# Kernel optimization log

Hardware: AMD Instinct MI355X
Metric: run time of the kernel (lower is better)

The kernel has to match this reference:

```python
import jax, jax.numpy as jnp
import numpy as np

B, CIN, COUT, T, F = 8, 64, 64, 512, 161
KH, KW = 3, 3
PAD_H, PAD_W = 1, 1
STRIDE_H, STRIDE_W = 1, 1
DIL_H, DIL_W = 1, 1


def setup_inputs() -> dict:
    key = jax.random.key(0)
    k1, k2, k3 = jax.random.split(key, 3)
    x = jax.random.normal(k1, (B, CIN, T, F), dtype=jnp.float32)
    # kernel: [out_ch, in_ch, kernels(freq), kH, kW]
    kernel = jax.random.normal(k2, (COUT, CIN, F, KH, KW), dtype=jnp.float32) * 0.05
    bias = jax.random.normal(k3, (1, COUT, 1, F), dtype=jnp.float32) * 0.05
    return {"x": x, "kernel": kernel, "bias": bias}


def reference(x, kernel, bias):
    # Frequency-varying conv: out[b,o,t,f] = sum_{i,m,n} xp[b,i,t*sH+m*dH, f*sW+n*dW] * kernel[o,i,f,m,n] + bias
    xp = jnp.pad(x, ((0, 0), (0, 0), (PAD_H, PAD_H), (PAD_W, PAD_W)))
    Hp, Wp = xp.shape[-2], xp.shape[-1]
    out_t = (Hp - ((KH - 1) * DIL_H + 1)) // STRIDE_H + 1
    out_f = (Wp - ((KW - 1) * DIL_W + 1)) // STRIDE_W + 1  # == F == kernels
    out = jnp.zeros((x.shape[0], kernel.shape[0], out_t, out_f), dtype=x.dtype)
    # Small fixed loop over the 3x3 window; avoids materializing [B,C,T,F,3,3] patches.
    for m in range(KH):
        for n in range(KW):
            xs = xp[:, :,
                    m * DIL_H : m * DIL_H + out_t * STRIDE_H : STRIDE_H,
                    n * DIL_W : n * DIL_W + out_f * STRIDE_W : STRIDE_W]  # [B,Cin,T,F]
            out = out + jnp.einsum('bitf,oif->botf', xs, kernel[:, :, :, m, n])
    out = out + bias
    return out
```

## Files before the change

### kernel.cpp

```cpp
#include <hip/hip_runtime.h>
#include <hip/hip_bf16.h>

#define CIN   64
#define COUT  64
#define TT    512
#define FF    161
#define KTOT  576
#define WST   (COUT*KTOT)
#define TFSTR (TT*FF)
#define FP_   168

#define W2_BYTES  ((size_t)FF*COUT*KTOT*2)
#define X2_BYTES  ((size_t)8*TT*FP_*64*2)
#define TMP_BYTES ((size_t)8*FF*TT*COUT*2)
#define PW_BLOCKS 5796

typedef __bf16 bf16x8 __attribute__((ext_vector_type(8)));
typedef float  f32x4  __attribute__((ext_vector_type(4)));
typedef unsigned short u16x8 __attribute__((ext_vector_type(8)));
typedef unsigned short u16x4 __attribute__((ext_vector_type(4)));
typedef unsigned int   u32x2 __attribute__((ext_vector_type(2)));
typedef float f4u __attribute__((ext_vector_type(4), aligned(4)));

__device__ __forceinline__ unsigned short f2bf(float v) {
    union { float f; unsigned int u; } c; c.f = v;
    unsigned int u = c.u + 0x7FFFu + ((c.u >> 16) & 1u);
    return (unsigned short)(u >> 16);
}
__device__ __forceinline__ float bf2f(unsigned short h) {
    union { unsigned int u; float f; } c; c.u = (unsigned)h << 16;
    return c.f;
}

__global__ __launch_bounds__(256) void prep_fused(
    const float* __restrict__ ksrc, unsigned short* __restrict__ w2,
    const float* __restrict__ x, unsigned short* __restrict__ x2)
{
    __shared__ unsigned short Xs[64][172];
    int bx = blockIdx.x;
    int tid = threadIdx.x;

    if (bx < PW_BLOCKS) {
        int g  = bx*256 + tid;
        int f  = g / 9216;
        int j  = g - f*9216;
        int o  = j / 144;
        int r  = j - o*144;
        int q  = r >> 4;
        int i4 = (r & 15) * 4;
        u16x4 v;
        #pragma unroll
        for (int e = 0; e < 4; ++e)
            v[e] = f2bf(ksrc[((size_t)(o*64 + i4 + e)*FF + f)*9 + q]);
        *(u16x4*)&w2[(size_t)f*36864 + j*4] = v;
        return;
    }

    int bt = bx - PW_BLOCKS;
    int b  = bt >> 9;
    int t  = bt & 511;
    const float* xb = x + (size_t)b*CIN*TFSTR + (size_t)t*FF;
    #pragma unroll
    for (int k = 0; k < 11; ++k) {
        int s = tid + k*256;
        if (s < 2624) {
            int i = s / 41;
            int u = s - i*41;
            const float* p = xb + (size_t)i*TFSTR + 4*u;
            if (u < 40) {
                f4u v = *(const f4u*)p;
                u32x2 pk = { (unsigned)f2bf(v.x) | ((unsigned)f2bf(v.y) << 16),
                             (unsigned)f2bf(v.z) | ((unsigned)f2bf(v.w) << 16) };
                *(u32x2*)&Xs[i][4*u] = pk;
            } else {
                Xs[i][160] = f2bf(*p);
            }
        }
    }
    __syncthreads();
    unsigned short* ob = x2 + (size_t)bt * FP_ * 64;
    #pragma unroll
    for (int k = 0; k < 6; ++k) {
        int s = tid + k*256;
        if (s < 1344) {
            int fp = s >> 3;
            int j  = s & 7;
            u16x8 v = {0,0,0,0,0,0,0,0};
            if (fp >= 1 && fp < 162) {
                int f = fp - 1;
                #pragma unroll
                for (int e = 0; e < 8; ++e) v[e] = Xs[j*8 + e][f];
            }
            *(u16x8*)&ob[fp*64 + j*8] = v;
        }
    }
}

__global__ __launch_bounds__(256, 4) void conv_mfma8(
    const unsigned short* __restrict__ x2, const unsigned short* __restrict__ w2,
    const float* __restrict__ bias, unsigned short* __restrict__ tmp)
{
    int bx   = blockIdx.x;
    int b    = bx & 7;
    int r    = bx >> 3;
    int tq   = r & 7;
    int fblk = r >> 3;
    int t0   = tq * 64;
    int f0   = fblk * 2;

    __shared__ alignas(16) unsigned short As[264*64];

    int tid = threadIdx.x;
    int wq  = tid >> 6;
    int l   = tid & 63;
    int l15 = l & 15;
    int lq  = l >> 4;
    int o   = wq*16 + l15;

    const unsigned short* zrow = x2 + 167*64;

    #pragma unroll
    for (int it = 0; it < 9; ++it) {
        int idx = tid + it*256;
        if (idx < 2112) {
            int row = idx >> 3;
            int j   = idx & 7;
            int fl  = row / 66;
            int tl  = row - fl*66;
            int gt  = t0 - 1 + tl;
            int fp  = f0 + fl;
            bool ok = (gt >= 0) && (gt < TT);
            int key = (tl + fl) & 7;
            const unsigned short* src = ok
                ? x2 + ((((size_t)b*TT + gt)*FP_ + fp)*64 + ((j ^ key) * 8))
                : zrow + j*8;
            __builtin_amdgcn_global_load_lds(
                (const __attribute__((address_space(1))) void*)src,
                (__attribute__((address_space(3))) void*)(As + (size_t)idx*8),
                16, 0, 0);
        }
    }
    __syncthreads();

    f32x4 acc[2][4] = {};
    const unsigned short* wb = w2 + ((size_t)f0*COUT + o)*KTOT;

    bf16x8 bw0[6], bw1[6];
    auto ldw = [&](bf16x8 (&dst)[6], int p) {
        int is = p / 3, dm = p - (p/3)*3;
        int kb = is*32 + lq*8;
        #pragma unroll
        for (int dn = 0; dn < 3; ++dn)
            #pragma unroll
            for (int u = 0; u < 2; ++u)
                dst[dn*2 + u] = *(const bf16x8*)&wb[(size_t)u*WST + (dm*3 + dn)*64 + kb];
    };

    ldw(bw0, 0);
    #pragma unroll
    for (int p = 0; p < 6; ++p) {
        if (p < 5) {
            if (p & 1) ldw(bw0, p + 1); else ldw(bw1, p + 1);
        }
        int is = p / 3, dm = p - (p/3)*3;
        int sbase = is*4 + lq;
        #pragma unroll
        for (int mf = 0; mf < 4; ++mf) {
            int tl = mf*16 + l15 + dm;
            bf16x8 a4[4];
            #pragma unroll
            for (int fl = 0; fl < 4; ++fl) {
                int slot = sbase ^ ((tl + fl) & 7);
                a4[fl] = *(const bf16x8*)&As[(size_t)(fl*66 + tl)*64 + slot*8];
            }
            #pragma unroll
            for (int dn = 0; dn < 3; ++dn)
                #pragma unroll
                for (int u = 0; u < 2; ++u)
                    acc[u][mf] = __builtin_amdgcn_mfma_f32_16x16x32_bf16(
                        a4[u + dn], (p & 1) ? bw1[dn*2 + u] : bw0[dn*2 + u],
                        acc[u][mf], 0, 0, 0);
        }
    }

    #pragma unroll
    for (int u = 0; u < 2; ++u) {
        int fe = f0 + u;
        if (fe < FF) {
            float bv = bias[o*FF + fe];
            size_t tb = ((size_t)b*FF + fe)*TT + t0;
            #pragma unroll
            for (int mf = 0; mf < 4; ++mf)
                #pragma unroll
                for (int rr = 0; rr < 4; ++rr) {
                    int t = mf*16 + lq*4 + rr;
                    tmp[(tb + t)*COUT + o] = f2bf(acc[u][mf][rr] + bv);
                }
        }
    }
}

__global__ __launch_bounds__(256) void finalize2(
    const unsigned short* __restrict__ tmp, float* __restrict__ out)
{
    int bx = blockIdx.x;
    int b  = bx & 7;
    int s  = bx >> 3;
    int tb = s >> 1;
    int oh = s & 1;
    int t0 = tb * 4;
    int o0 = oh * 32;

    __shared__ unsigned short Ld[644*40];

    int tid = threadIdx.x;

    #pragma unroll
    for (int k = 0; k < 11; ++k) {
        int sl = tid + k*256;
        if (sl < 2576) {
            int f = sl >> 4;
            int r = sl & 15;
            int t = r >> 2;
            int j = r & 3;
            const unsigned short* src =
                tmp + (((size_t)b*FF + f)*TT + t0 + t)*COUT + o0 + j*8;
            int row = t*FF + f;
            *(u16x8*)&Ld[row*40 + ((j ^ (f & 3)) << 3)] = *(const u16x8*)src;
        }
    }
    __syncthreads();

    for (int ol = 0; ol < 32; ++ol) {
        int o = o0 + ol;
        float* op = out + (((size_t)b*COUT + o)*TT + t0)*FF;
        int jo = ol >> 3, o7 = ol & 7;
        #pragma unroll
        for (int k = 0; k < 3; ++k) {
            int r = tid + k*256;
            if (r < 4*FF) {
                int f = r % FF;
                op[r] = bf2f(Ld[r*40 + ((jo ^ (f & 3)) << 3) + o7]);
            }
        }
    }
}

__global__ __launch_bounds__(256) void conv_mfma(
    const float* __restrict__ x, const unsigned short* __restrict__ w2,
    const float* __restrict__ bias, float* __restrict__ out)
{
    int bx = blockIdx.x;
    int r  = bx & 7;
    int q  = bx >> 3;
    int fblk = q % 41;
    int g  = (q / 41) * 8 + r;
    int b  = g >> 3;
    int t0 = (g & 7) * 64;
    int f0 = fblk * 4;

    __shared__ unsigned short Bs[6][66][64];
    int tid = threadIdx.x;

    for (int i = 0; i < 64; i += 4) {
        #pragma unroll
        for (int pp = 0; pp < 2; ++pp) {
            int p = tid + pp*256;
            if (p < 396) {
                int tl = p / 6, fl = p % 6;
                int gt = t0 - 1 + tl;
                int gf = f0 - 1 + fl;
                bool ok = (gt >= 0) && (gt < TT) && (gf >= 0) && (gf < FF);
                const float* xp = x + (((size_t)(b*CIN + i)*TT + gt)*FF + gf);
                float v0 = ok ? xp[0]       : 0.f;
                float v1 = ok ? xp[TFSTR]   : 0.f;
                float v2 = ok ? xp[2*TFSTR] : 0.f;
                float v3 = ok ? xp[3*TFSTR] : 0.f;
                int isw = i ^ (((tl + fl) & 7) << 3);
                ushort4 pk;
                pk.x = f2bf(v0); pk.y = f2bf(v1); pk.z = f2bf(v2); pk.w = f2bf(v3);
                *reinterpret_cast<ushort4*>(&Bs[fl][tl][isw]) = pk;
            }
        }
    }
    __syncthreads();

    int wv = tid >> 6;
    int l  = tid & 63;
    int f  = f0 + wv;
    if (f >= FF) return;

    int l15 = l & 15;
    int lq  = l >> 4;
    f32x4 acc[4][4] = {};
    const unsigned short* wb = w2 + (size_t)f * (COUT * KTOT);

    #pragma unroll
    for (int dm = 0; dm < 3; ++dm)
    #pragma unroll
    for (int dn = 0; dn < 3; ++dn) {
        int fl = wv + dn;
        int kq = (dm*3 + dn) * 64;
        #pragma unroll
        for (int is = 0; is < 2; ++is) {
            int i0 = is*32 + lq*8;
            bf16x8 a[4];
            #pragma unroll
            for (int mf = 0; mf < 4; ++mf) {
                int tl  = mf*16 + l15 + dm;
                int isw = i0 ^ (((tl + fl) & 7) << 3);
                a[mf] = *(const bf16x8*)&Bs[fl][tl][isw];
            }
            int kb = kq + i0;
            #pragma unroll
            for (int nf = 0; nf < 4; ++nf) {
                bf16x8 bfr = *(const bf16x8*)&wb[(size_t)(nf*16 + l15) * KTOT + kb];
                #pragma unroll
                for (int mf = 0; mf < 4; ++mf)
                    acc[mf][nf] = __builtin_amdgcn_mfma_f32_16x16x32_bf16(
                        a[mf], bfr, acc[mf][nf], 0, 0, 0);
            }
        }
    }

    #pragma unroll
    for (int nf = 0; nf < 4; ++nf) {
        int o = nf*16 + l15;
        float bv = bias[o*FF + f];
        size_t obase = (((size_t)b*COUT + o)*TT + t0 + lq*4)*FF + f;
        #pragma unroll
        for (int mf = 0; mf < 4; ++mf)
            #pragma unroll
            for (int rr = 0; rr < 4; ++rr)
                out[obase + (size_t)(mf*16 + rr)*FF] = acc[mf][nf][rr] + bv;
    }
}

extern "C" void kernel_launch(void* const* d_in, const int* in_sizes, int n_in,
                              void* d_out, int out_size, void* d_ws, size_t ws_size,
                              hipStream_t stream)
{
    (void)in_sizes; (void)n_in; (void)out_size;
    const float* x    = (const float*)d_in[0];
    const float* k    = (const float*)d_in[1];
    const float* bias = (const float*)d_in[2];
    float* out = (float*)d_out;
    unsigned short* w2  = (unsigned short*)d_ws;
    unsigned short* x2  = (unsigned short*)((char*)d_ws + W2_BYTES);
    unsigned short* tmp = (unsigned short*)((char*)d_ws + W2_BYTES + X2_BYTES);

    bool big2 = (ws_size >= W2_BYTES + X2_BYTES + TMP_BYTES);

    prep_fused<<<big2 ? (PW_BLOCKS + 8*TT) : PW_BLOCKS, 256, 0, stream>>>(k, w2, x, x2);

    if (big2) {
        conv_mfma8<<<5184, 256, 0, stream>>>(x2, w2, bias, tmp);
        finalize2<<<2048, 256, 0, stream>>>(tmp, out);
    } else {
        conv_mfma<<<8*41*8, 256, 0, stream>>>(x, w2, bias, out);
    }
}
```

Baseline: 261.1 us.

## Switch conv to 32x32x16 MFMA tiles and stage weight repack through LDS

The conv kernel now gives each wave one frequency and 32 output channels, and uses 32x32x16 bf16 MFMA over the nine taps, where it used 16x16x32 across two frequencies. This changes the LDS A-fragment reuse and the accumulator layout. The weight-prep blocks now read contiguous rows of the kernel into shared memory and write out the transposed bf16 layout. This replaces scattered strided global reads with far fewer blocks. The larger MFMA shape may shift register pressure and occupancy.

```diff
diff --git a/kernel.cpp b/kernel.cpp
--- a/kernel.cpp
+++ b/kernel.cpp
@@ -13,10 +13,11 @@
 #define W2_BYTES  ((size_t)FF*COUT*KTOT*2)
 #define X2_BYTES  ((size_t)8*TT*FP_*64*2)
 #define TMP_BYTES ((size_t)8*FF*TT*COUT*2)
-#define PW_BLOCKS 5796
+#define PREPW_BLOCKS 512
 
 typedef __bf16 bf16x8 __attribute__((ext_vector_type(8)));
 typedef float  f32x4  __attribute__((ext_vector_type(4)));
+typedef float  f32x16 __attribute__((ext_vector_type(16)));
 typedef unsigned short u16x8 __attribute__((ext_vector_type(8)));
 typedef unsigned short u16x4 __attribute__((ext_vector_type(4)));
 typedef unsigned int   u32x2 __attribute__((ext_vector_type(2)));
@@ -32,31 +33,45 @@
     return c.f;
 }
 
-__global__ __launch_bounds__(256) void prep_fused(
+__global__ __launch_bounds__(256) void prep_fused2(
     const float* __restrict__ ksrc, unsigned short* __restrict__ w2,
     const float* __restrict__ x, unsigned short* __restrict__ x2)
 {
+    __shared__ unsigned short Ls[64*190];
     __shared__ unsigned short Xs[64][172];
     int bx = blockIdx.x;
     int tid = threadIdx.x;
 
-    if (bx < PW_BLOCKS) {
-        int g  = bx*256 + tid;
-        int f  = g / 9216;
-        int j  = g - f*9216;
-        int o  = j / 144;
-        int r  = j - o*144;
-        int q  = r >> 4;
-        int i4 = (r & 15) * 4;
-        u16x4 v;
-        #pragma unroll
-        for (int e = 0; e < 4; ++e)
-            v[e] = f2bf(ksrc[((size_t)(o*64 + i4 + e)*FF + f)*9 + q]);
-        *(u16x4*)&w2[(size_t)f*36864 + j*4] = v;
+    if (bx < PREPW_BLOCKS) {
+        int o  = bx >> 3;
+        int c  = bx & 7;
+        int f0 = c * 21;
+        int nf = (c == 7) ? 14 : 21;
+        int nr = nf * 9;
+        const float* src = ksrc + (size_t)o*64*FF*9 + f0*9;
+        int tot = 64 * nr;
+        for (int e = tid; e < tot; e += 256) {
+            int i  = e / nr;
+            int rr = e - i*nr;
+            Ls[i*190 + rr] = f2bf(src[(size_t)i*FF*9 + rr]);
+        }
+        __syncthreads();
+        unsigned short* dst = w2 + (size_t)f0*WST + o*KTOT;
+        int wt = nf * 144;
+        for (int w = tid; w < wt; w += 256) {
+            int fl = w / 144;
+            int rr = w - fl*144;
+            int q  = rr >> 4;
+            int i0 = (rr & 15) * 4;
+            u16x4 v;
+            #pragma unroll
+            for (int e = 0; e < 4; ++e) v[e] = Ls[(i0 + e)*190 + fl*9 + q];
+            *(u16x4*)&dst[(size_t)fl*WST + q*64 + i0] = v;
+        }
         return;
     }
 
-    int bt = bx - PW_BLOCKS;
+    int bt = bx - PREPW_BLOCKS;
     int b  = bt >> 9;
     int t  = bt & 511;
     const float* xb = x + (size_t)b*CIN*TFSTR + (size_t)t*FF;
@@ -96,7 +111,7 @@
     }
 }
 
-__global__ __launch_bounds__(256, 4) void conv_mfma8(
+__global__ __launch_bounds__(256, 4) void conv_mfma10(
     const unsigned short* __restrict__ x2, const unsigned short* __restrict__ w2,
     const float* __restrict__ bias, unsigned short* __restrict__ tmp)
 {
@@ -113,9 +128,11 @@
     int tid = threadIdx.x;
     int wq  = tid >> 6;
     int l   = tid & 63;
-    int l15 = l & 15;
-    int lq  = l >> 4;
-    int o   = wq*16 + l15;
+    int l31 = l & 31;
+    int lh  = l >> 5;
+    int f   = f0 + (wq >> 1);
+    int o   = (wq & 1)*32 + l31;
+    int flb = wq >> 1;
 
     const unsigned short* zrow = x2 + 167*64;
 
@@ -142,60 +159,45 @@
     }
     __syncthreads();
 
-    f32x4 acc[2][4] = {};
-    const unsigned short* wb = w2 + ((size_t)f0*COUT + o)*KTOT;
-
-    bf16x8 bw0[6], bw1[6];
-    auto ldw = [&](bf16x8 (&dst)[6], int p) {
-        int is = p / 3, dm = p - (p/3)*3;
-        int kb = is*32 + lq*8;
-        #pragma unroll
-        for (int dn = 0; dn < 3; ++dn)
-            #pragma unroll
-            for (int u = 0; u < 2; ++u)
-                dst[dn*2 + u] = *(const bf16x8*)&wb[(size_t)u*WST + (dm*3 + dn)*64 + kb];
+    f32x16 acc0 = {}, acc1 = {};
+    const unsigned short* wb = w2 + ((size_t)f*COUT + o)*KTOT + lh*8;
+
+    bf16x8 bwA[4], bwB[4];
+    auto ldw = [&](bf16x8 (&dst)[4], int t9) {
+        #pragma unroll
+        for (int ks = 0; ks < 4; ++ks)
+            dst[ks] = *(const bf16x8*)&wb[t9*64 + ks*16];
     };
 
-    ldw(bw0, 0);
-    #pragma unroll
-    for (int p = 0; p < 6; ++p) {
-        if (p < 5) {
-            if (p & 1) ldw(bw0, p + 1); else ldw(bw1, p + 1);
-        }
-        int is = p / 3, dm = p - (p/3)*3;
-        int sbase = is*4 + lq;
-        #pragma unroll
-        for (int mf = 0; mf < 4; ++mf) {
-            int tl = mf*16 + l15 + dm;
-            bf16x8 a4[4];
-            #pragma unroll
-            for (int fl = 0; fl < 4; ++fl) {
-                int slot = sbase ^ ((tl + fl) & 7);
-                a4[fl] = *(const bf16x8*)&As[(size_t)(fl*66 + tl)*64 + slot*8];
-            }
-            #pragma unroll
-            for (int dn = 0; dn < 3; ++dn)
-                #pragma unroll
-                for (int u = 0; u < 2; ++u)
-                    acc[u][mf] = __builtin_amdgcn_mfma_f32_16x16x32_bf16(
-                        a4[u + dn], (p & 1) ? bw1[dn*2 + u] : bw0[dn*2 + u],
-                        acc[u][mf], 0, 0, 0);
-        }
-    }
-
-    #pragma unroll
-    for (int u = 0; u < 2; ++u) {
-        int fe = f0 + u;
-        if (fe < FF) {
-            float bv = bias[o*FF + fe];
-            size_t tb = ((size_t)b*FF + fe)*TT + t0;
-            #pragma unroll
-            for (int mf = 0; mf < 4; ++mf)
-                #pragma unroll
-                for (int rr = 0; rr < 4; ++rr) {
-                    int t = mf*16 + lq*4 + rr;
-                    tmp[(tb + t)*COUT + o] = f2bf(acc[u][mf][rr] + bv);
-                }
+    ldw(bwA, 0);
+    #pragma unroll
+    for (int t9 = 0; t9 < 9; ++t9) {
+        if (t9 < 8) { if (t9 & 1) ldw(bwA, t9 + 1); else ldw(bwB, t9 + 1); }
+        int dm = t9 / 3, dn = t9 - dm*3;
+        int fl = flb + dn;
+        #pragma unroll
+        for (int ks = 0; ks < 4; ++ks) {
+            int sb = ks*2 + lh;
+            int tlA = l31 + dm;
+            int slA = sb ^ ((tlA + fl) & 7);
+            bf16x8 a0 = *(const bf16x8*)&As[(size_t)(fl*66 + tlA)*64 + slA*8];
+            int tlB = 32 + l31 + dm;
+            int slB = sb ^ ((tlB + fl) & 7);
+            bf16x8 a1 = *(const bf16x8*)&As[(size_t)(fl*66 + tlB)*64 + slB*8];
+            bf16x8 bw = (t9 & 1) ? bwB[ks] : bwA[ks];
+            acc0 = __builtin_amdgcn_mfma_f32_32x32x16_bf16(a0, bw, acc0, 0, 0, 0);
+            acc1 = __builtin_amdgcn_mfma_f32_32x32x16_bf16(a1, bw, acc1, 0, 0, 0);
+        }
+    }
+
+    if (f < FF) {
+        float bv = bias[o*FF + f];
+        size_t tb = ((size_t)b*FF + f)*TT + t0;
+        #pragma unroll
+        for (int reg = 0; reg < 16; ++reg) {
+            int t = (reg & 3) + 8*(reg >> 2) + 4*lh;
+            tmp[(tb + t)*COUT + o]      = f2bf(acc0[reg] + bv);
+            tmp[(tb + t + 32)*COUT + o] = f2bf(acc1[reg] + bv);
         }
     }
 }
@@ -351,12 +353,12 @@
 
     bool big2 = (ws_size >= W2_BYTES + X2_BYTES + TMP_BYTES);
 
-    prep_fused<<<big2 ? (PW_BLOCKS + 8*TT) : PW_BLOCKS, 256, 0, stream>>>(k, w2, x, x2);
-
     if (big2) {
-        conv_mfma8<<<5184, 256, 0, stream>>>(x2, w2, bias, tmp);
+        prep_fused2<<<PREPW_BLOCKS + 8*TT, 256, 0, stream>>>(k, w2, x, x2);
+        conv_mfma10<<<5184, 256, 0, stream>>>(x2, w2, bias, tmp);
         finalize2<<<2048, 256, 0, stream>>>(tmp, out);
     } else {
+        prep_fused2<<<PREPW_BLOCKS, 256, 0, stream>>>(k, w2, x, x2);
         conv_mfma<<<8*41*8, 256, 0, stream>>>(x, w2, bias, out);
     }
 }
```

Result: slower. 293.4 us (+12.4%).

## Make conv blocks persistent over several frequency pairs with ring-buffered input planes

Applied to the files above, without the earlier changes.

Each conv block now handles 2-3 consecutive frequency pairs instead of one. Input planes sit in a 6-slot LDS ring, so the two planes shared by adjacent pairs are reused and the next pair's planes are prefetched while the current pair computes. This cuts redundant global loads of the overlapping padded-frequency planes and reduces the grid from 5184 to 2048 blocks. In exchange LDS use per block grows, occupancy drops to 3 blocks per CU, and extra barriers are added between iterations.

```diff
diff --git a/kernel.cpp b/kernel.cpp
--- a/kernel.cpp
+++ b/kernel.cpp
@@ -21,6 +21,7 @@
 typedef unsigned short u16x4 __attribute__((ext_vector_type(4)));
 typedef unsigned int   u32x2 __attribute__((ext_vector_type(2)));
 typedef float f4u __attribute__((ext_vector_type(4), aligned(4)));
+typedef float f2u __attribute__((ext_vector_type(2), aligned(4)));
 
 __device__ __forceinline__ unsigned short f2bf(float v) {
     union { float f; unsigned int u; } c; c.f = v;
@@ -96,19 +97,20 @@
     }
 }
 
-__global__ __launch_bounds__(256, 4) void conv_mfma8(
+__global__ __launch_bounds__(256, 3) void conv_mfma11(
     const unsigned short* __restrict__ x2, const unsigned short* __restrict__ w2,
     const float* __restrict__ bias, unsigned short* __restrict__ tmp)
 {
-    int bx   = blockIdx.x;
-    int b    = bx & 7;
-    int r    = bx >> 3;
-    int tq   = r & 7;
-    int fblk = r >> 3;
-    int t0   = tq * 64;
-    int f0   = fblk * 2;
-
-    __shared__ alignas(16) unsigned short As[264*64];
+    int bx  = blockIdx.x;
+    int b   = bx & 7;
+    int s   = bx >> 3;
+    int tq  = s & 7;
+    int seg = s >> 3;
+    int fb0   = (seg < 17) ? seg*3 : 51 + (seg - 17)*2;
+    int niter = (seg < 17) ? 3 : 2;
+    int t0  = tq * 64;
+
+    __shared__ alignas(16) unsigned short As[6*4224];
 
     int tid = threadIdx.x;
     int wq  = tid >> 6;
@@ -119,84 +121,102 @@
 
     const unsigned short* zrow = x2 + 167*64;
 
-    #pragma unroll
-    for (int it = 0; it < 9; ++it) {
-        int idx = tid + it*256;
-        if (idx < 2112) {
-            int row = idx >> 3;
-            int j   = idx & 7;
-            int fl  = row / 66;
-            int tl  = row - fl*66;
-            int gt  = t0 - 1 + tl;
-            int fp  = f0 + fl;
-            bool ok = (gt >= 0) && (gt < TT);
-            int key = (tl + fl) & 7;
-            const unsigned short* src = ok
-                ? x2 + ((((size_t)b*TT + gt)*FP_ + fp)*64 + ((j ^ key) * 8))
-                : zrow + j*8;
-            __builtin_amdgcn_global_load_lds(
-                (const __attribute__((address_space(1))) void*)src,
-                (__attribute__((address_space(3))) void*)(As + (size_t)idx*8),
-                16, 0, 0);
-        }
-    }
+    auto stage_plane = [&](int fp) {
+        unsigned short* dstb = As + (fp % 6)*4224;
+        #pragma unroll
+        for (int it = 0; it < 3; ++it) {
+            int idx = tid + it*256;
+            if (idx < 528) {
+                int row = idx >> 3;
+                int j   = idx & 7;
+                int gt  = t0 - 1 + row;
+                bool ok = (gt >= 0) && (gt < TT);
+                int key = (row + fp) & 7;
+                const unsigned short* src = ok
+                    ? x2 + ((((size_t)b*TT + gt)*FP_ + fp)*64 + ((j ^ key)*8))
+                    : zrow + j*8;
+                __builtin_amdgcn_global_load_lds(
+                    (const __attribute__((address_space(1))) void*)src,
+                    (__attribute__((address_space(3))) void*)(dstb + (size_t)idx*8),
+                    16, 0, 0);
+            }
+        }
+    };
+
+    #pragma unroll
+    for (int q = 0; q < 4; ++q) stage_plane(fb0*2 + q);
     __syncthreads();
 
-    f32x4 acc[2][4] = {};
-    const unsigned short* wb = w2 + ((size_t)f0*COUT + o)*KTOT;
-
-    bf16x8 bw0[6], bw1[6];
-    auto ldw = [&](bf16x8 (&dst)[6], int p) {
-        int is = p / 3, dm = p - (p/3)*3;
-        int kb = is*32 + lq*8;
-        #pragma unroll
-        for (int dn = 0; dn < 3; ++dn)
-            #pragma unroll
-            for (int u = 0; u < 2; ++u)
-                dst[dn*2 + u] = *(const bf16x8*)&wb[(size_t)u*WST + (dm*3 + dn)*64 + kb];
-    };
-
-    ldw(bw0, 0);
-    #pragma unroll
-    for (int p = 0; p < 6; ++p) {
-        if (p < 5) {
-            if (p & 1) ldw(bw0, p + 1); else ldw(bw1, p + 1);
-        }
-        int is = p / 3, dm = p - (p/3)*3;
-        int sbase = is*4 + lq;
-        #pragma unroll
-        for (int mf = 0; mf < 4; ++mf) {
-            int tl = mf*16 + l15 + dm;
-            bf16x8 a4[4];
-            #pragma unroll
-            for (int fl = 0; fl < 4; ++fl) {
-                int slot = sbase ^ ((tl + fl) & 7);
-                a4[fl] = *(const bf16x8*)&As[(size_t)(fl*66 + tl)*64 + slot*8];
-            }
+    for (int n = 0; n < niter; ++n) {
+        int f0 = (fb0 + n)*2;
+        if (n + 1 < niter) {
+            stage_plane(f0 + 4);
+            stage_plane(f0 + 5);
+        }
+
+        f32x4 acc[2][4] = {};
+        const unsigned short* wb = w2 + ((size_t)f0*COUT + o)*KTOT;
+
+        int ps[4], kf[4];
+        #pragma unroll
+        for (int fl = 0; fl < 4; ++fl) {
+            ps[fl] = ((f0 + fl) % 6) * 4224;
+            kf[fl] = (f0 + fl) & 7;
+        }
+
+        bf16x8 bw0[6], bw1[6];
+        auto ldw = [&](bf16x8 (&dst)[6], int p) {
+            int is = p / 3, dm = p - (p/3)*3;
+            int kb = is*32 + lq*8;
             #pragma unroll
             for (int dn = 0; dn < 3; ++dn)
                 #pragma unroll
                 for (int u = 0; u < 2; ++u)
-                    acc[u][mf] = __builtin_amdgcn_mfma_f32_16x16x32_bf16(
-                        a4[u + dn], (p & 1) ? bw1[dn*2 + u] : bw0[dn*2 + u],
-                        acc[u][mf], 0, 0, 0);
-        }
-    }
-
-    #pragma unroll
-    for (int u = 0; u < 2; ++u) {
-        int fe = f0 + u;
-        if (fe < FF) {
-            float bv = bias[o*FF + fe];
-            size_t tb = ((size_t)b*FF + fe)*TT + t0;
-            #pragma unroll
-            for (int mf = 0; mf < 4; ++mf)
-                #pragma unroll
-                for (int rr = 0; rr < 4; ++rr) {
-                    int t = mf*16 + lq*4 + rr;
-                    tmp[(tb + t)*COUT + o] = f2bf(acc[u][mf][rr] + bv);
+                    dst[dn*2 + u] = *(const bf16x8*)&wb[(size_t)u*WST + (dm*3+dn)*64 + kb];
+        };
+
+        ldw(bw0, 0);
+        #pragma unroll
+        for (int p = 0; p < 6; ++p) {
+            if (p < 5) { if (p & 1) ldw(bw0, p + 1); else ldw(bw1, p + 1); }
+            int dm = p - (p/3)*3;
+            int sbase = (p/3)*4 + lq;
+            #pragma unroll
+            for (int mf = 0; mf < 4; ++mf) {
+                int tl = mf*16 + l15 + dm;
+                bf16x8 a4[4];
+                #pragma unroll
+                for (int fl = 0; fl < 4; ++fl) {
+                    int phys = sbase ^ ((tl + kf[fl]) & 7);
+                    a4[fl] = *(const bf16x8*)&As[ps[fl] + tl*64 + phys*8];
                 }
-        }
+                #pragma unroll
+                for (int dn = 0; dn < 3; ++dn)
+                    #pragma unroll
+                    for (int u = 0; u < 2; ++u)
+                        acc[u][mf] = __builtin_amdgcn_mfma_f32_16x16x32_bf16(
+                            a4[u + dn], (p & 1) ? bw1[dn*2 + u] : bw0[dn*2 + u],
+                            acc[u][mf], 0, 0, 0);
+            }
+        }
+
+        #pragma unroll
+        for (int u = 0; u < 2; ++u) {
+            int fe = f0 + u;
+            if (fe < FF) {
+                float bv = bias[o*FF + fe];
+                size_t tb = ((size_t)b*FF + fe)*TT + t0;
+                #pragma unroll
+                for (int mf = 0; mf < 4; ++mf)
+                    #pragma unroll
+                    for (int rr = 0; rr < 4; ++rr) {
+                        int t = mf*16 + lq*4 + rr;
+                        tmp[(tb + t)*COUT + o] = f2bf(acc[u][mf][rr] + bv);
+                    }
+            }
+        }
+
+        if (n + 1 < niter) __syncthreads();
     }
 }
 
@@ -354,7 +374,7 @@
     prep_fused<<<big2 ? (PW_BLOCKS + 8*TT) : PW_BLOCKS, 256, 0, stream>>>(k, w2, x, x2);
 
     if (big2) {
-        conv_mfma8<<<5184, 256, 0, stream>>>(x2, w2, bias, tmp);
+        conv_mfma11<<<2048, 256, 0, stream>>>(x2, w2, bias, tmp);
         finalize2<<<2048, 256, 0, stream>>>(tmp, out);
     } else {
         conv_mfma<<<8*41*8, 256, 0, stream>>>(x, w2, bias, out);
```

Result: no change. 264.8 us (+1.4%).
